# Optimization experiments

Measured on AMD Instinct MI355X. Metric: run time of the kernel, lower is better.

## Reference

```python
import jax, jax.numpy as jnp
import numpy as np

HEAD = 64

PARAM_NAMES = ['x_r','x_w','x_k','x_v','x_a','x_g','w0','w1','w2','a0','a1','a2',
               'v0','v1','v2','g1','g2','k_k','k_a','r_k','W_r','W_k','W_v','W_o',
               'ln_x_w','ln_x_b','ln1_w','ln1_b','ln2_w','ln2_b','c_x_k','W_ck','W_cv']


def token_shift(x):
    # previous token, zero-padded at t=0 (stateless shift state)
    return jnp.pad(x, ((0, 0), (1, 0), (0, 0)))[:, :-1]


def layer_norm(x, w, b, eps=1e-5):
    m = jnp.mean(x, -1, keepdims=True)
    v = jnp.mean(jnp.square(x - m), -1, keepdims=True)
    return (x - m) * jax.lax.rsqrt(v + eps) * w + b


def group_norm_heads(x, w, b, H, eps=64e-5):
    # GroupNorm(H, C) as used by RWKV7 ln_x (eps = head_size * 1e-5)
    B, T, C = x.shape
    xh = x.reshape(B, T, H, C // H)
    m = jnp.mean(xh, -1, keepdims=True)
    v = jnp.mean(jnp.square(xh - m), -1, keepdims=True)
    xh = (xh - m) * jax.lax.rsqrt(v + eps)
    return xh.reshape(B, T, C) * w + b


def wkv7(r, w, k, v, a, b):
    # r,w,k,v,a,b: [B,T,H,N]; w is per-channel decay in (0,1)
    # S_t = S_{t-1} * diag(w_t) + (S_{t-1} @ a_t) b_t^T + v_t k_t^T ; y_t = S_t @ r_t
    B, T, H, N = r.shape
    def step(S, inp):
        r_t, w_t, k_t, v_t, a_t, b_t = inp
        sa = jnp.einsum('bhij,bhj->bhi', S, a_t)
        S = S * w_t[:, :, None, :] + sa[..., None] * b_t[:, :, None, :] + v_t[..., None] * k_t[:, :, None, :]
        y = jnp.einsum('bhij,bhj->bhi', S, r_t)
        return S, y
    xs = tuple(jnp.moveaxis(t, 1, 0) for t in (r, w, k, v, a, b))
    S0 = jnp.zeros((B, H, N, N), r.dtype)
    _, ys = jax.lax.scan(step, S0, xs)
    return jnp.moveaxis(ys, 0, 1)


def time_mix(x, v_first, p, is_first_layer):
    B, T, C = x.shape
    H, N = C // HEAD, HEAD
    xx = token_shift(x) - x
    xr = x + xx * p['x_r']; xw = x + xx * p['x_w']; xk = x + xx * p['x_k']
    xv = x + xx * p['x_v']; xa = x + xx * p['x_a']; xg = x + xx * p['x_g']
    r = xr @ p['W_r']
    w = -jax.nn.softplus(-(p['w0'] + jnp.tanh(xw @ p['w1']) @ p['w2'])) - 0.5
    k = xk @ p['W_k']
    v = xv @ p['W_v']
    if is_first_layer:
        v_first = v
    else:
        v = v + (v_first - v) * jax.nn.sigmoid(p['v0'] + (xv @ p['v1']) @ p['v2'])
    a = jax.nn.sigmoid(p['a0'] + (xa @ p['a1']) @ p['a2'])  # in-context learning rate
    g = jax.nn.sigmoid(xg @ p['g1']) @ p['g2']
    kk = (k * p['k_k']).reshape(B, T, H, N)
    kk = kk / jnp.maximum(jnp.linalg.norm(kk, axis=-1, keepdims=True), 1e-12)
    k = k * (1.0 + (a - 1.0) * p['k_a'])
    decay = jnp.exp(-jnp.exp(w)).reshape(B, T, H, N)
    rh = r.reshape(B, T, H, N)
    kh = k.reshape(B, T, H, N)
    vh = v.reshape(B, T, H, N)
    ah = a.reshape(B, T, H, N)
    y = wkv7(rh, decay, kh, vh, -kk, kk * ah).reshape(B, T, C)
    y = group_norm_heads(y, p['ln_x_w'], p['ln_x_b'], H)
    bonus = jnp.sum(rh * kh * p['r_k'], -1, keepdims=True) * vh
    y = y + bonus.reshape(B, T, C)
    return (y * g) @ p['W_o'], v_first


def channel_mix(x, p):
    xx = token_shift(x) - x
    k = x + xx * p['c_x_k']
    k = jnp.square(jax.nn.relu(k @ p['W_ck']))
    return k @ p['W_cv']


def encoder_forward(x, params):
    L = params['W_r'].shape[0]
    v_first = None
    for i in range(L):
        p = {n: params[n][i] for n in PARAM_NAMES}
        att, v_first = time_mix(layer_norm(x, p['ln1_w'], p['ln1_b']), v_first, p, i == 0)
        x = x + att
        x = x + channel_mix(layer_norm(x, p['ln2_w'], p['ln2_b']), p)
    return x


def setup_inputs() -> dict:
    key = jax.random.key(0)
    L, B, T, C = 6, 2, 512, 768
    H, N = C // HEAD, HEAD
    Dw, Da, Dv, Dg, F = 64, 64, 32, 128, 4 * C
    keys = iter(jax.random.split(key, 48))
    def rn(shape, s):
        return jax.random.normal(next(keys), shape, jnp.float32) * s
    def ru(shape):
        return jax.random.uniform(next(keys), shape, jnp.float32)
    inp = {
        'x': rn((B, T, C), 1.0),
        'x_r': ru((L, C)), 'x_w': ru((L, C)), 'x_k': ru((L, C)),
        'x_v': ru((L, C)), 'x_a': ru((L, C)), 'x_g': ru((L, C)),
        'w0': rn((L, C), 0.3), 'w1': rn((L, C, Dw), 0.02), 'w2': rn((L, Dw, C), 0.02),
        'a0': rn((L, C), 0.1), 'a1': rn((L, C, Da), 0.02), 'a2': rn((L, Da, C), 0.02),
        'v0': rn((L, C), 0.1), 'v1': rn((L, C, Dv), 0.02), 'v2': rn((L, Dv, C), 0.02),
        'g1': rn((L, C, Dg), 0.02), 'g2': rn((L, Dg, C), 0.02),
        'k_k': 0.85 + rn((L, C), 0.05), 'k_a': 1.0 + rn((L, C), 0.05),
        'r_k': rn((L, H, N), 0.1),
        'W_r': rn((L, C, C), 0.02), 'W_k': rn((L, C, C), 0.02),
        'W_v': rn((L, C, C), 0.02), 'W_o': rn((L, C, C), 0.02),
        'ln_x_w': 1.0 + rn((L, C), 0.05), 'ln_x_b': rn((L, C), 0.05),
        'ln1_w': 1.0 + rn((L, C), 0.05), 'ln1_b': rn((L, C), 0.05),
        'ln2_w': 1.0 + rn((L, C), 0.05), 'ln2_b': rn((L, C), 0.05),
        'c_x_k': ru((L, C)),
        'W_ck': rn((L, C, F), 0.02), 'W_cv': rn((L, F, C), 0.02),
    }
    return inp


def reference(x, x_r, x_w, x_k, x_v, x_a, x_g, w0, w1, w2, a0, a1, a2, v0, v1, v2,
              g1, g2, k_k, k_a, r_k, W_r, W_k, W_v, W_o, ln_x_w, ln_x_b,
              ln1_w, ln1_b, ln2_w, ln2_b, c_x_k, W_ck, W_cv):
    params = dict(zip(PARAM_NAMES, (x_r, x_w, x_k, x_v, x_a, x_g, w0, w1, w2, a0, a1, a2,
                                    v0, v1, v2, g1, g2, k_k, k_a, r_k, W_r, W_k, W_v, W_o,
                                    ln_x_w, ln_x_b, ln1_w, ln1_b, ln2_w, ln2_b, c_x_k, W_ck, W_cv)))
    return encoder_forward(x, params)
```

## Files before the change

### kernel.cpp

```cpp
#include <hip/hip_runtime.h>
#include <hip/hip_bf16.h>
#include <math.h>

#define LAYERS 6
#define BBATCH 2
#define TT 512
#define CC 768
#define HH 12
#define MT (BBATCH*TT)
#define FF (4*CC)
#define LCH 32
#define NC (TT/LCH)
#define BH (BBATCH*HH)
#define SPAD 65

typedef __hip_bfloat16 bf16;
typedef __bf16 bf16x8 __attribute__((ext_vector_type(8)));
typedef __bf16 bf16x4 __attribute__((ext_vector_type(4)));
typedef float f32x4 __attribute__((ext_vector_type(4)));

__device__ inline bf16 f2b(float f) { return __float2bfloat16(f); }
__device__ inline __bf16 f2bb(float f) {
    __hip_bfloat16 h = __float2bfloat16(f);
    return __builtin_bit_cast(__bf16, h);
}
__device__ inline float bb2f(__bf16 h) {
    return __bfloat162float(__builtin_bit_cast(__hip_bfloat16, h));
}


__global__ __launch_bounds__(256) void copy_f(float* __restrict__ dst, const float* __restrict__ src) {
    size_t i = (size_t)blockIdx.x * 256 + threadIdx.x;
    dst[i] = src[i];
}


__global__ __launch_bounds__(256) void ln_shift_kernel(const float* __restrict__ x,
                                                       const float* __restrict__ w,
                                                       const float* __restrict__ b,
                                                       bf16* __restrict__ out) {
    int row = blockIdx.x;
    int t = row % TT;
    const float* xr = x + (size_t)row * CC;
    const float* xp = xr - CC;
    int tid = threadIdx.x;
    float c0 = xr[tid], c1 = xr[tid + 256], c2 = xr[tid + 512];
    float p0 = 0.f, p1 = 0.f, p2 = 0.f;
    if (t > 0) { p0 = xp[tid]; p1 = xp[tid + 256]; p2 = xp[tid + 512]; }
    float s  = c0 + c1 + c2, q  = c0 * c0 + c1 * c1 + c2 * c2;
    float sp = p0 + p1 + p2, qp = p0 * p0 + p1 * p1 + p2 * p2;
    for (int m = 1; m < 64; m <<= 1) {
        s += __shfl_xor(s, m); q += __shfl_xor(q, m);
        sp += __shfl_xor(sp, m); qp += __shfl_xor(qp, m);
    }
    __shared__ float rs[4], rq[4], rsp[4], rqp[4];
    int wid = tid >> 6;
    if ((tid & 63) == 0) { rs[wid] = s; rq[wid] = q; rsp[wid] = sp; rqp[wid] = qp; }
    __syncthreads();
    s  = rs[0] + rs[1] + rs[2] + rs[3];   q  = rq[0] + rq[1] + rq[2] + rq[3];
    sp = rsp[0] + rsp[1] + rsp[2] + rsp[3]; qp = rqp[0] + rqp[1] + rqp[2] + rqp[3];
    float meanC = s * (1.f / CC);
    float invC  = rsqrtf(q * (1.f / CC) - meanC * meanC + 1e-5f);
    float meanP = sp * (1.f / CC);
    float invP  = rsqrtf(qp * (1.f / CC) - meanP * meanP + 1e-5f);
    bf16* orow = out + (size_t)row * 1536;
    float cv[3] = {c0, c1, c2};
    float pv[3] = {p0, p1, p2};
#pragma unroll
    for (int j = 0; j < 3; ++j) {
        int cc = tid + j * 256;
        float lnc = (cv[j] - meanC) * invC * w[cc] + b[cc];
        float lnp = (t > 0) ? (pv[j] - meanP) * invP * w[cc] + b[cc] : 0.f;
        orow[cc] = f2b(lnc);
        orow[768 + cc] = f2b(lnp - lnc);
    }
}


struct CEntry { const float* W; const float* mix; bf16* dst; int Ksrc, Nsrc, Npad, Kdst, bstart; };
struct CArgs { CEntry e[14]; };

__global__ __launch_bounds__(256) void convert_weights(CArgs ca) {
    int bid = blockIdx.x;
    int idx = 0;
#pragma unroll
    for (int i = 1; i < 14; ++i) if (bid >= ca.e[i].bstart) idx = i;
    CEntry E = ca.e[idx];
    int t = bid - E.bstart;
    int ntN = E.Npad >> 5;
    int tn = (t % ntN) * 32, tk = (t / ntN) * 32;
    __shared__ float tile[32][33];
    int c = threadIdx.x & 31, r0 = threadIdx.x >> 5;
    int ks = tk;
    const float* mixp = nullptr;
    if (tk >= E.Ksrc) { ks = tk - E.Ksrc; mixp = E.mix; }
#pragma unroll
    for (int i = 0; i < 4; ++i) {
        int r = r0 + i * 8;
        float v = (tn + c < E.Nsrc) ? E.W[(size_t)(ks + r) * E.Nsrc + tn + c] : 0.f;
        if (mixp) v *= mixp[ks + r];
        tile[r][c] = v;
    }
    __syncthreads();
#pragma unroll
    for (int i = 0; i < 4; ++i) {
        int r = r0 + i * 8;
        E.dst[(size_t)(tn + r) * E.Kdst + tk + c] = f2b(tile[c][r]);
    }
}


struct EpiG {
    float* outF; bf16* outH;
    const float* p1; const float* p2;
    int epi, ld, ntrue;
};
struct EpiArgs { EpiG g[7]; int nb[8]; };

__device__ inline void epi_store(const EpiG& E, size_t idx, int lc, float v) {
    switch (E.epi) {
        case 0: E.outF[idx] = v; break;
        case 1: E.outH[idx] = f2b(v); break;
        case 2: E.outH[idx] = f2b(tanhf(v)); break;
        case 3: E.outH[idx] = f2b(1.f / (1.f + expf(-v))); break;
        case 4: { float t = fmaxf(v, 0.f); E.outH[idx] = f2b(t * t); } break;
        case 5: E.outF[idx] += v; break;
        case 6: { float z = E.p1[lc] + v; float nz = -z;
                  float sp = (nz > 20.f) ? nz : log1pf(expf(nz));
                  E.outF[idx] = expf(-expf(-sp - 0.5f)); } break;
        case 7: E.outF[idx] = 1.f / (1.f + expf(-(E.p1[lc] + v))); break;
        case 8: { float vv = E.outF[idx];
                  float s = 1.f / (1.f + expf(-(E.p1[lc] + v)));
                  E.outF[idx] = vv + (E.p2[idx] - vv) * s; } break;
    }
}


template<int BM, int BN>
__global__ __launch_bounds__(256) void gemm_multi(const __bf16* __restrict__ A,
                                                  const __bf16* __restrict__ Bt,
                                                  int K, EpiArgs ea) {
    constexpr int FM = BM / 32, FN = BN / 32;
    constexpr int ABYTES = BM * 64;
    constexpr int TOT = (BM + BN) * 64;
    constexpr int NCHUNK = TOT / 4096;
    __shared__ __align__(16) char smem[2][TOT];
    int tid = threadIdx.x;
    int lane = tid & 63, wid = tid >> 6;
    int bm = blockIdx.y * BM, bn = blockIdx.x * BN;
    int wm = (wid >> 1) * (BM / 2), wn = (wid & 1) * (BN / 2);
    f32x4 acc[FM][FN];
#pragma unroll
    for (int i = 0; i < FM; ++i)
#pragma unroll
        for (int j = 0; j < FN; ++j) acc[i][j] = (f32x4){0.f, 0.f, 0.f, 0.f};

    int nk = K >> 5;
    auto stage = [&](int buf, int k0) {
        char* sb = &smem[buf][0];
#pragma unroll
        for (int c = 0; c < NCHUNK; ++c) {
            int d = c * 4096 + tid * 16;
            int isB = d >= ABYTES;
            int dd = isB ? d - ABYTES : d;
            int row = dd >> 6;
            int u = (dd >> 4) & 3;
            int su = u ^ (row & 3);
            const __bf16* src = isB ? (Bt + (size_t)(bn + row) * K + k0 + su * 8)
                                    : (A  + (size_t)(bm + row) * K + k0 + su * 8);
            char* ldst = sb + c * 4096 + (tid & 192) * 16;
            __builtin_amdgcn_global_load_lds(
                (const __attribute__((address_space(1))) unsigned int*)src,
                (__attribute__((address_space(3))) unsigned int*)ldst, 16, 0, 0);
        }
    };

    stage(0, 0);
    __syncthreads();
    for (int t = 0; t < nk; ++t) {
        if (t + 1 < nk) stage((t + 1) & 1, (t + 1) * 32);
        const char* sA = &smem[t & 1][0];
        const char* sB = &smem[t & 1][ABYTES];
        int u = lane >> 4, r0 = lane & 15;
        bf16x8 af[FM], bfr[FN];
#pragma unroll
        for (int i = 0; i < FM; ++i) {
            int row = wm + i * 16 + r0;
            int su = u ^ (row & 3);
            af[i] = *(const bf16x8*)(sA + row * 64 + su * 16);
        }
#pragma unroll
        for (int j = 0; j < FN; ++j) {
            int row = wn + j * 16 + r0;
            int su = u ^ (row & 3);
            bfr[j] = *(const bf16x8*)(sB + row * 64 + su * 16);
        }
#pragma unroll
        for (int i = 0; i < FM; ++i)
#pragma unroll
            for (int j = 0; j < FN; ++j)
                acc[i][j] = __builtin_amdgcn_mfma_f32_16x16x32_bf16(af[i], bfr[j], acc[i][j], 0, 0, 0);
        __syncthreads();
    }

    int gid = 0;
#pragma unroll 1
    while (bn >= ea.nb[gid + 1]) ++gid;
    EpiG E = ea.g[gid];
    int colBase = ea.nb[gid];
#pragma unroll
    for (int i = 0; i < FM; ++i) {
#pragma unroll
        for (int j = 0; j < FN; ++j) {
#pragma unroll
            for (int q = 0; q < 4; ++q) {
                int gm = bm + wm + i * 16 + (lane >> 4) * 4 + q;
                int lc = bn + wn + j * 16 + (lane & 15) - colBase;
                if (lc < E.ntrue)
                    epi_store(E, (size_t)gm * E.ld + lc, lc, acc[i][j][q]);
            }
        }
    }
}


struct G2G { const __bf16* A; const __bf16* Bt; float* outF; const float* p1; const float* p2; int K; int epi; };
struct G2Args { G2G g[4]; };

template<int BM, int BN>
__global__ __launch_bounds__(256) void gemm_g2(G2Args ga) {
    G2G G = ga.g[blockIdx.z];
    const __bf16* A = G.A;
    const __bf16* Bt = G.Bt;
    int K = G.K;
    constexpr int FM = BM / 32, FN = BN / 32;
    constexpr int ABYTES = BM * 64;
    constexpr int TOT = (BM + BN) * 64;
    constexpr int NCHUNK = TOT / 4096;
    __shared__ __align__(16) char smem[2][TOT];
    int tid = threadIdx.x;
    int lane = tid & 63, wid = tid >> 6;
    int bm = blockIdx.y * BM, bn = blockIdx.x * BN;
    int wm = (wid >> 1) * (BM / 2), wn = (wid & 1) * (BN / 2);
    f32x4 acc[FM][FN];
#pragma unroll
    for (int i = 0; i < FM; ++i)
#pragma unroll
        for (int j = 0; j < FN; ++j) acc[i][j] = (f32x4){0.f, 0.f, 0.f, 0.f};

    int nk = K >> 5;
    auto stage = [&](int buf, int k0) {
        char* sb = &smem[buf][0];
#pragma unroll
        for (int c = 0; c < NCHUNK; ++c) {
            int d = c * 4096 + tid * 16;
            int isB = d >= ABYTES;
            int dd = isB ? d - ABYTES : d;
            int row = dd >> 6;
            int u = (dd >> 4) & 3;
            int su = u ^ (row & 3);
            const __bf16* src = isB ? (Bt + (size_t)(bn + row) * K + k0 + su * 8)
                                    : (A  + (size_t)(bm + row) * K + k0 + su * 8);
            char* ldst = sb + c * 4096 + (tid & 192) * 16;
            __builtin_amdgcn_global_load_lds(
                (const __attribute__((address_space(1))) unsigned int*)src,
                (__attribute__((address_space(3))) unsigned int*)ldst, 16, 0, 0);
        }
    };

    stage(0, 0);
    __syncthreads();
    for (int t = 0; t < nk; ++t) {
        if (t + 1 < nk) stage((t + 1) & 1, (t + 1) * 32);
        const char* sA = &smem[t & 1][0];
        const char* sB = &smem[t & 1][ABYTES];
        int u = lane >> 4, r0 = lane & 15;
        bf16x8 af[FM], bfr[FN];
#pragma unroll
        for (int i = 0; i < FM; ++i) {
            int row = wm + i * 16 + r0;
            int su = u ^ (row & 3);
            af[i] = *(const bf16x8*)(sA + row * 64 + su * 16);
        }
#pragma unroll
        for (int j = 0; j < FN; ++j) {
            int row = wn + j * 16 + r0;
            int su = u ^ (row & 3);
            bfr[j] = *(const bf16x8*)(sB + row * 64 + su * 16);
        }
#pragma unroll
        for (int i = 0; i < FM; ++i)
#pragma unroll
            for (int j = 0; j < FN; ++j)
                acc[i][j] = __builtin_amdgcn_mfma_f32_16x16x32_bf16(af[i], bfr[j], acc[i][j], 0, 0, 0);
        __syncthreads();
    }

    EpiG E;
    E.outF = G.outF; E.outH = nullptr; E.p1 = G.p1; E.p2 = G.p2;
    E.epi = G.epi; E.ld = 768; E.ntrue = 768;
#pragma unroll
    for (int i = 0; i < FM; ++i) {
#pragma unroll
        for (int j = 0; j < FN; ++j) {
#pragma unroll
            for (int q = 0; q < 4; ++q) {
                int gm = bm + wm + i * 16 + (lane >> 4) * 4 + q;
                int lc = bn + wn + j * 16 + (lane & 15);
                epi_store(E, (size_t)gm * 768 + lc, lc, acc[i][j][q]);
            }
        }
    }
}


__global__ __launch_bounds__(256) void chunkA_kernel(
    const float* __restrict__ r, const float* __restrict__ wd,
    const float* __restrict__ kraw, const float* __restrict__ av_,
    const float* __restrict__ v,
    const float* __restrict__ kkw, const float* __restrict__ kaw,
    float* __restrict__ kupd,
    float* __restrict__ yintra, float* __restrict__ zrO,
    __bf16* __restrict__ mtHi, __bf16* __restrict__ mtLo,
    float* __restrict__ zcO) {
    int c = blockIdx.x, bh = blockIdx.y;
    int b = bh / HH, h = bh % HH;
    __shared__ float Di[LCH][SPAD];
    __shared__ float Ah[LCH][SPAD];
    __shared__ float Bh[LCH][SPAD];
    __shared__ float Kh[LCH][SPAD];
    __shared__ float Rh[LCH][SPAD];
    __shared__ float Vt[LCH][SPAD];
    __shared__ float Qm[LCH][SPAD];
    __shared__ float Gba[LCH][LCH], Gka[LCH][LCH], Grb[LCH][LCH], Grk[LCH][LCH];
    int tid = threadIdx.x;
    int n = tid & 63, tq = tid >> 6;
    size_t base = ((size_t)(b * TT + c * LCH)) * CC + h * 64 + n;
    int cvec = h * 64 + n;
    float kkwv = kkw[cvec], kawv = kaw[cvec];
#pragma unroll
    for (int e = 0; e < 8; ++e) {
        int t = tq * 8 + e;
        size_t off = base + (size_t)t * CC;
        float kr = kraw[off];
        float aval = av_[off];
        float kk0 = kr * kkwv;
        float ss = kk0 * kk0;
        for (int m = 1; m < 64; m <<= 1) ss += __shfl_xor(ss, m);
        float rinv = 1.f / fmaxf(sqrtf(ss), 1e-12f);
        float kkv = kk0 * rinv;
        float ku = kr * (1.f + (aval - 1.f) * kawv);
        kupd[off] = ku;
        Di[t][n] = wd[off];
        Ah[t][n] = -kkv;
        Bh[t][n] = kkv * aval;
        Kh[t][n] = ku;
        Rh[t][n] = r[off];
        Vt[t][n] = v[off];
    }
    __syncthreads();
    if (tid < 64) {
        float d = 1.f;
        for (int t = 0; t < LCH; ++t) { d *= Di[t][tid]; Di[t][tid] = d; }
    }
    __syncthreads();
#pragma unroll
    for (int e = 0; e < 8; ++e) {
        int t = tq * 8 + e;
        float di = Di[t][n];
        float dp = (t == 0) ? 1.f : Di[t - 1][n];
        float inv = 1.f / di;
        Ah[t][n] *= dp;
        Bh[t][n] *= inv;
        Kh[t][n] *= inv;
        Rh[t][n] *= di;
    }
    __syncthreads();
    {
        int tp = tid >> 4, sp = tid & 15;
        int t0 = 2 * tp, s0 = 2 * sp;
        float gba00 = 0.f, gba01 = 0.f, gba10 = 0.f, gba11 = 0.f;
        float gka00 = 0.f, gka01 = 0.f, gka10 = 0.f, gka11 = 0.f;
        float grb00 = 0.f, grb01 = 0.f, grb10 = 0.f, grb11 = 0.f;
        float grk00 = 0.f, grk01 = 0.f, grk10 = 0.f, grk11 = 0.f;
#pragma unroll 4
        for (int j = 0; j < 64; ++j) {
            float a0 = Ah[t0][j], a1 = Ah[t0 + 1][j];
            float r0 = Rh[t0][j], r1 = Rh[t0 + 1][j];
            float b0 = Bh[s0][j], b1 = Bh[s0 + 1][j];
            float k0 = Kh[s0][j], k1 = Kh[s0 + 1][j];
            gba00 = fmaf(a0, b0, gba00); gba01 = fmaf(a0, b1, gba01);
            gba10 = fmaf(a1, b0, gba10); gba11 = fmaf(a1, b1, gba11);
            gka00 = fmaf(a0, k0, gka00); gka01 = fmaf(a0, k1, gka01);
            gka10 = fmaf(a1, k0, gka10); gka11 = fmaf(a1, k1, gka11);
            grb00 = fmaf(r0, b0, grb00); grb01 = fmaf(r0, b1, grb01);
            grb10 = fmaf(r1, b0, grb10); grb11 = fmaf(r1, b1, grb11);
            grk00 = fmaf(r0, k0, grk00); grk01 = fmaf(r0, k1, grk01);
            grk10 = fmaf(r1, k0, grk10); grk11 = fmaf(r1, k1, grk11);
        }
#pragma unroll
        for (int dt = 0; dt < 2; ++dt) {
            int t = t0 + dt;
#pragma unroll
            for (int ds = 0; ds < 2; ++ds) {
                int s = s0 + ds;
                float vba = dt ? (ds ? gba11 : gba10) : (ds ? gba01 : gba00);
                float vka = dt ? (ds ? gka11 : gka10) : (ds ? gka01 : gka00);
                float vrb = dt ? (ds ? grb11 : grb10) : (ds ? grb01 : grb00);
                float vrk = dt ? (ds ? grk11 : grk10) : (ds ? grk01 : grk00);
                Gba[t][s] = (s < t)  ? vba : 0.f;
                Gka[t][s] = (s < t)  ? vka : 0.f;
                Grb[t][s] = (s <= t) ? vrb : 0.f;
                Grk[t][s] = (s <= t) ? vrk : 0.f;
            }
        }
    }
    __syncthreads();
    {
        float acc[8];
#pragma unroll
        for (int e = 0; e < 8; ++e) acc[e] = 0.f;
        for (int s = 0; s < LCH; ++s) {
            float vs = Vt[s][n];
#pragma unroll
            for (int e = 0; e < 8; ++e)
                acc[e] = fmaf(Gka[tq * 8 + e][s], vs, acc[e]);
        }
#pragma unroll
        for (int e = 0; e < 8; ++e) Qm[tq * 8 + e][n] = acc[e];
    }
    __syncthreads();
    if (tq == 0) {
        for (int t = 1; t < LCH; ++t) {
            float acc = Ah[t][n];
            for (int s = 0; s < t; ++s) acc = fmaf(Gba[t][s], Ah[s][n], acc);
            Ah[t][n] = acc;
        }
    } else if (tq == 1) {
        for (int t = 1; t < LCH; ++t) {
            float acc = Qm[t][n];
            for (int s = 0; s < t; ++s) acc = fmaf(Gba[t][s], Qm[s][n], acc);
            Qm[t][n] = acc;
        }
    }
    __syncthreads();
    size_t obase = ((size_t)(bh * NC + c)) * LCH * 64;
    {
        float accY[8], accZ[8];
#pragma unroll
        for (int e = 0; e < 8; ++e) { accY[e] = 0.f; accZ[e] = Rh[tq * 8 + e][n]; }
        for (int s = 0; s < LCH; ++s) {
            float vs = Vt[s][n], qs = Qm[s][n], us = Ah[s][n];
#pragma unroll
            for (int e = 0; e < 8; ++e) {
                int t = tq * 8 + e;
                float grk_ = Grk[t][s], grb_ = Grb[t][s];
                accY[e] = fmaf(grk_, vs, fmaf(grb_, qs, accY[e]));
                accZ[e] = fmaf(grb_, us, accZ[e]);
            }
        }
#pragma unroll
        for (int e = 0; e < 8; ++e) {
            int t = tq * 8 + e;
            yintra[obase + t * 64 + n] = accY[e];
            zrO[obase + t * 64 + n] = accZ[e];
        }
    }
    {
        int pi = tid >> 4, ni = tid & 15;
        float accM[4][4], accZc[4][4];
#pragma unroll
        for (int dp = 0; dp < 4; ++dp)
#pragma unroll
            for (int dn = 0; dn < 4; ++dn) { accM[dp][dn] = 0.f; accZc[dp][dn] = 0.f; }
        for (int s = 0; s < LCH; ++s) {
            float aa[4], vv[4], qq[4], bb[4], kk[4];
#pragma unroll
            for (int d = 0; d < 4; ++d) {
                aa[d] = Ah[s][4 * pi + d];
                vv[d] = Vt[s][4 * pi + d];
                qq[d] = Qm[s][4 * pi + d];
                bb[d] = Bh[s][4 * ni + d];
                kk[d] = Kh[s][4 * ni + d];
            }
#pragma unroll
            for (int dp = 0; dp < 4; ++dp)
#pragma unroll
                for (int dn = 0; dn < 4; ++dn) {
                    accM[dp][dn]  = fmaf(aa[dp], bb[dn], accM[dp][dn]);
                    accZc[dp][dn] = fmaf(vv[dp], kk[dn], fmaf(qq[dp], bb[dn], accZc[dp][dn]));
                }
        }
        size_t mbase = ((size_t)(bh * NC + c)) * 4096;
        float dl[4];
#pragma unroll
        for (int dn = 0; dn < 4; ++dn) dl[dn] = Di[LCH - 1][4 * ni + dn];
#pragma unroll
        for (int dp = 0; dp < 4; ++dp) {
            int p = 4 * pi + dp;
            f32x4 z4;
#pragma unroll
            for (int dn = 0; dn < 4; ++dn) z4[dn] = dl[dn] * accZc[dp][dn];
            *(f32x4*)(zcO + mbase + p * 64 + 4 * ni) = z4;
        }
#pragma unroll
        for (int dn = 0; dn < 4; ++dn) {
            int nn = 4 * ni + dn;
            float dlv = dl[dn];
            bf16x4 h4, l4;
#pragma unroll
            for (int dp = 0; dp < 4; ++dp) {
                int p = 4 * pi + dp;
                float mm = (accM[dp][dn] + ((p == nn) ? 1.f : 0.f)) * dlv;
                __bf16 hb = f2bb(mm);
                h4[dp] = hb;
                l4[dp] = f2bb(mm - bb2f(hb));
            }
            *(bf16x4*)(mtHi + mbase + (size_t)nn * 64 + 4 * pi) = h4;
            *(bf16x4*)(mtLo + mbase + (size_t)nn * 64 + 4 * pi) = l4;
        }
    }
}


__global__ __launch_bounds__(256) void chunkB1_kernel(
    const float* __restrict__ zc,
    const __bf16* __restrict__ mtHi,
    const __bf16* __restrict__ mtLo,
    float* __restrict__ schk) {
    int bh = blockIdx.x;
    int tid = threadIdx.x;
    int lane = tid & 63, w = tid >> 6;
    int r0 = lane & 15, u = lane >> 4;
    __shared__ __align__(16) float S[64][68];
    for (int i = tid; i < 64 * 68; i += 256) (&S[0][0])[i] = 0.f;
    const float* zbase = zc + (size_t)bh * NC * 4096;
    const __bf16* hbase = mtHi + (size_t)bh * NC * 4096;
    const __bf16* lbase = mtLo + (size_t)bh * NC * 4096;
    float* sbase = schk + (size_t)bh * NC * 4096;
    int arow = w * 16 + r0;

    bf16x8 mh[2][4][2], ml[2][4][2];
    f32x4 zf[2][4];
#pragma unroll
    for (int ct = 0; ct < 4; ++ct) {
#pragma unroll
        for (int ks = 0; ks < 2; ++ks) {
            size_t mo = (size_t)(ct * 16 + r0) * 64 + ks * 32 + u * 8;
            mh[0][ct][ks] = *(const bf16x8*)(hbase + mo);
            ml[0][ct][ks] = *(const bf16x8*)(lbase + mo);
        }
#pragma unroll
        for (int q = 0; q < 4; ++q)
            zf[0][ct][q] = zbase[(size_t)(w * 16 + u * 4 + q) * 64 + ct * 16 + r0];
    }
    __syncthreads();
#pragma unroll
    for (int c = 0; c < NC - 1; ++c) {
        constexpr int dummy = 0; (void)dummy;
        const int cb = c & 1;
        if (c + 1 < NC - 1) {
            const __bf16* hn = hbase + (size_t)(c + 1) * 4096;
            const __bf16* ln = lbase + (size_t)(c + 1) * 4096;
            const float* zn = zbase + (size_t)(c + 1) * 4096;
#pragma unroll
            for (int ct = 0; ct < 4; ++ct) {
#pragma unroll
                for (int ks = 0; ks < 2; ++ks) {
                    size_t mo = (size_t)(ct * 16 + r0) * 64 + ks * 32 + u * 8;
                    mh[cb ^ 1][ct][ks] = *(const bf16x8*)(hn + mo);
                    ml[cb ^ 1][ct][ks] = *(const bf16x8*)(ln + mo);
                }
#pragma unroll
                for (int q = 0; q < 4; ++q)
                    zf[cb ^ 1][ct][q] = zn[(size_t)(w * 16 + u * 4 + q) * 64 + ct * 16 + r0];
            }
        }
        bf16x8 ah[2], al[2];
#pragma unroll
        for (int ks = 0; ks < 2; ++ks) {
            f32x4 s0 = *(const f32x4*)&S[arow][ks * 32 + u * 8];
            f32x4 s1 = *(const f32x4*)&S[arow][ks * 32 + u * 8 + 4];
#pragma unroll
            for (int e = 0; e < 4; ++e) {
                __bf16 h0 = f2bb(s0[e]);
                ah[ks][e] = h0;
                al[ks][e] = f2bb(s0[e] - bb2f(h0));
                __bf16 h1 = f2bb(s1[e]);
                ah[ks][4 + e] = h1;
                al[ks][4 + e] = f2bb(s1[e] - bb2f(h1));
            }
        }
        f32x4 acc[4];
#pragma unroll
        for (int ct = 0; ct < 4; ++ct) {
            acc[ct] = zf[cb][ct];
#pragma unroll
            for (int ks = 0; ks < 2; ++ks) {
                acc[ct] = __builtin_amdgcn_mfma_f32_16x16x32_bf16(ah[ks], mh[cb][ct][ks], acc[ct], 0, 0, 0);
                acc[ct] = __builtin_amdgcn_mfma_f32_16x16x32_bf16(ah[ks], ml[cb][ct][ks], acc[ct], 0, 0, 0);
                acc[ct] = __builtin_amdgcn_mfma_f32_16x16x32_bf16(al[ks], mh[cb][ct][ks], acc[ct], 0, 0, 0);
            }
        }
        __syncthreads();
        float* cp = sbase + (size_t)(c + 1) * 4096;
#pragma unroll
        for (int ct = 0; ct < 4; ++ct) {
#pragma unroll
            for (int q = 0; q < 4; ++q) {
                int row = w * 16 + u * 4 + q;
                int col = ct * 16 + r0;
                S[row][col] = acc[ct][q];
                cp[(size_t)row * 64 + col] = acc[ct][q];
            }
        }
        __syncthreads();
    }
}


__global__ __launch_bounds__(256) void chunkY_kernel(
    const float* __restrict__ yintra, const float* __restrict__ zrI,
    const float* __restrict__ schk,
    const float* __restrict__ r, const float* __restrict__ kupd,
    const float* __restrict__ v, const float* __restrict__ g,
    const float* __restrict__ rk, const float* __restrict__ lw,
    const float* __restrict__ lb, bf16* __restrict__ out) {
    int c = blockIdx.x, bh = blockIdx.y;
    int b = bh / HH, h = bh % HH;
    __shared__ float Y[LCH][SPAD];
    __shared__ float Zr[LCH][SPAD];
    __shared__ float Sh[64][SPAD];
    int tid = threadIdx.x;
    int n = tid & 63, tq = tid >> 6;
    size_t obase = ((size_t)(bh * NC + c)) * LCH * 64;
#pragma unroll
    for (int e = 0; e < 8; ++e) {
        int idx = tid + e * 256;
        int row = idx >> 6, col = idx & 63;
        Y[row][col] = yintra[obase + idx];
        Zr[row][col] = zrI[obase + idx];
    }
    if (c > 0) {
        size_t sbase = ((size_t)(bh * NC + c)) * 4096;
#pragma unroll
        for (int e = 0; e < 16; ++e) {
            int idx = tid + e * 256;
            Sh[idx >> 6][idx & 63] = schk[sbase + idx];
        }
    }
    __syncthreads();
    if (c > 0) {
        float acc[8];
#pragma unroll
        for (int e = 0; e < 8; ++e) acc[e] = 0.f;
        for (int p = 0; p < 64; ++p) {
            float sv = Sh[n][p];
#pragma unroll
            for (int e = 0; e < 8; ++e)
                acc[e] = fmaf(Zr[tq * 8 + e][p], sv, acc[e]);
        }
#pragma unroll
        for (int e = 0; e < 8; ++e) Y[tq * 8 + e][n] += acc[e];
    }
    size_t rowbase = ((size_t)(b * TT + c * LCH)) * CC + h * 64 + n;
    float rkv = rk[h * 64 + n];
    float lwv = lw[h * 64 + n], lbv = lb[h * 64 + n];
#pragma unroll
    for (int e = 0; e < 8; ++e) {
        int t = tq * 8 + e;
        size_t off = rowbase + (size_t)t * CC;
        float yv = Y[t][n];
        float rv = r[off], kv = kupd[off], vv = v[off];
        float s1 = yv, s2 = yv * yv, s3 = rv * kv * rkv;
        for (int m = 1; m < 64; m <<= 1) {
            s1 += __shfl_xor(s1, m);
            s2 += __shfl_xor(s2, m);
            s3 += __shfl_xor(s3, m);
        }
        float mean = s1 * (1.f / 64.f);
        float var  = s2 * (1.f / 64.f) - mean * mean;
        float inv  = rsqrtf(var + 64e-5f);
        float val  = (yv - mean) * inv * lwv + lbv + s3 * vv;
        out[off] = f2b(val * g[off]);
    }
}


extern "C" void kernel_launch(void* const* d_in, const int* in_sizes, int n_in,
                              void* d_out, int out_size, void* d_ws, size_t ws_size,
                              hipStream_t stream) {
    (void)in_sizes; (void)n_in; (void)out_size;
    const float* x    = (const float*)d_in[0];
    const float* x_r  = (const float*)d_in[1];
    const float* x_w  = (const float*)d_in[2];
    const float* x_k  = (const float*)d_in[3];
    const float* x_v  = (const float*)d_in[4];
    const float* x_a  = (const float*)d_in[5];
    const float* x_g  = (const float*)d_in[6];
    const float* w0   = (const float*)d_in[7];
    const float* w1   = (const float*)d_in[8];
    const float* w2   = (const float*)d_in[9];
    const float* a0   = (const float*)d_in[10];
    const float* a1   = (const float*)d_in[11];
    const float* a2   = (const float*)d_in[12];
    const float* v0   = (const float*)d_in[13];
    const float* v1   = (const float*)d_in[14];
    const float* v2   = (const float*)d_in[15];
    const float* g1   = (const float*)d_in[16];
    const float* g2   = (const float*)d_in[17];
    const float* k_k  = (const float*)d_in[18];
    const float* k_a  = (const float*)d_in[19];
    const float* r_k  = (const float*)d_in[20];
    const float* W_r  = (const float*)d_in[21];
    const float* W_k  = (const float*)d_in[22];
    const float* W_v  = (const float*)d_in[23];
    const float* W_o  = (const float*)d_in[24];
    const float* ln_x_w = (const float*)d_in[25];
    const float* ln_x_b = (const float*)d_in[26];
    const float* ln1_w  = (const float*)d_in[27];
    const float* ln1_b  = (const float*)d_in[28];
    const float* ln2_w  = (const float*)d_in[29];
    const float* ln2_b  = (const float*)d_in[30];
    const float* c_x_k  = (const float*)d_in[31];
    const float* W_ck   = (const float*)d_in[32];
    const float* W_cv   = (const float*)d_in[33];

    const size_t MC = (size_t)MT * CC;
    char* wsb = (char*)d_ws;
    size_t woff = 0;
    auto alloc = [&](size_t bytes) -> void* {
        void* p = wsb + woff;
        woff += (bytes + 255) & ~(size_t)255;
        return p;
    };
    bf16* Bcat  = (bf16*)alloc((size_t)2624 * 1536 * 2);
    bf16* Bck   = (bf16*)alloc((size_t)3072 * 1536 * 2);
    bf16* w2t   = (bf16*)alloc((size_t)768 * 64 * 2);
    bf16* a2t   = (bf16*)alloc((size_t)768 * 64 * 2);
    bf16* v2t   = (bf16*)alloc((size_t)768 * 32 * 2);
    bf16* g2t   = (bf16*)alloc((size_t)768 * 128 * 2);
    bf16* Wo_t  = (bf16*)alloc((size_t)768 * 768 * 2);
    bf16* Wcv_t = (bf16*)alloc((size_t)768 * 3072 * 2);
    bf16* A1    = (bf16*)alloc((size_t)MT * 1536 * 2);
    float* rbuf  = (float*)alloc(MC * 4);
    float* kraw  = (float*)alloc(MC * 4);
    float* kupd  = (float*)alloc(MC * 4);
    float* vbuf  = (float*)alloc(MC * 4);
    float* vfirst= (float*)alloc(MC * 4);
    float* abuf  = (float*)alloc(MC * 4);
    float* dbuf  = (float*)alloc(MC * 4);
    float* gbuf  = (float*)alloc(MC * 4);
    bf16* w1o   = (bf16*)alloc((size_t)MT * 64 * 2);
    bf16* a1o   = (bf16*)alloc((size_t)MT * 64 * 2);
    bf16* v1o   = (bf16*)alloc((size_t)MT * 32 * 2);
    bf16* g1o   = (bf16*)alloc((size_t)MT * 128 * 2);
    bf16* hbuf  = (bf16*)alloc((size_t)MT * FF * 2);
    bf16* ghout = (bf16*)alloc(MC * 2);
    float* yintraW = (float*)alloc((size_t)BH * NC * LCH * 64 * 4);
    float* zrW     = (float*)alloc((size_t)BH * NC * LCH * 64 * 4);
    __bf16* mtHiW  = (__bf16*)alloc((size_t)BH * NC * 4096 * 2);
    __bf16* mtLoW  = (__bf16*)alloc((size_t)BH * NC * 4096 * 2);
    float* zcW     = (float*)alloc((size_t)BH * NC * 4096 * 4);
    float* schkW   = (float*)alloc((size_t)BH * NC * 4096 * 4);
    if (woff > ws_size) return;

    float* xcur = (float*)d_out;
    copy_f<<<MC / 256, 256, 0, stream>>>(xcur, x);

    for (int l = 0; l < LAYERS; ++l) {
        size_t oC = (size_t)l * CC;
        float* vptr = (l == 0) ? vfirst : vbuf;

        CArgs ca;
        ca.e[0]  = {W_r  + (size_t)l * 589824, x_r + oC, Bcat,               768, 768, 768, 1536, 0};
        ca.e[1]  = {W_k  + (size_t)l * 589824, x_k + oC, Bcat + (size_t)768  * 1536, 768, 768, 768, 1536, 0};
        ca.e[2]  = {W_v  + (size_t)l * 589824, x_v + oC, Bcat + (size_t)1536 * 1536, 768, 768, 768, 1536, 0};
        ca.e[3]  = {w1   + (size_t)l * 49152,  x_w + oC, Bcat + (size_t)2304 * 1536, 768, 64, 64, 1536, 0};
        ca.e[4]  = {a1   + (size_t)l * 49152,  x_a + oC, Bcat + (size_t)2368 * 1536, 768, 64, 64, 1536, 0};
        ca.e[5]  = {g1   + (size_t)l * 98304,  x_g + oC, Bcat + (size_t)2432 * 1536, 768, 128, 128, 1536, 0};
        ca.e[6]  = {v1   + (size_t)l * 24576,  x_v + oC, Bcat + (size_t)2560 * 1536, 768, 32, 64, 1536, 0};
        ca.e[7]  = {W_ck + (size_t)l * 2359296, c_x_k + oC, Bck, 768, 3072, 3072, 1536, 0};
        ca.e[8]  = {w2   + (size_t)l * 49152,  nullptr, w2t,   64, 768, 768, 64, 0};
        ca.e[9]  = {a2   + (size_t)l * 49152,  nullptr, a2t,   64, 768, 768, 64, 0};
        ca.e[10] = {v2   + (size_t)l * 24576,  nullptr, v2t,   32, 768, 768, 32, 0};
        ca.e[11] = {g2   + (size_t)l * 98304,  nullptr, g2t,  128, 768, 768, 128, 0};
        ca.e[12] = {W_o  + (size_t)l * 589824, nullptr, Wo_t, 768, 768, 768, 768, 0};
        ca.e[13] = {W_cv + (size_t)l * 2359296, nullptr, Wcv_t, 3072, 768, 768, 3072, 0};
        int btot = 0;
        for (int i = 0; i < 14; ++i) {
            ca.e[i].bstart = btot;
            btot += (ca.e[i].Npad >> 5) * (ca.e[i].Kdst >> 5);
        }
        convert_weights<<<btot, 256, 0, stream>>>(ca);

        ln_shift_kernel<<<MT, 256, 0, stream>>>(xcur, ln1_w + oC, ln1_b + oC, A1);

        EpiArgs e1;
        e1.g[0] = {rbuf,  nullptr, nullptr, nullptr, 0, 768, 768};
        e1.g[1] = {kraw,  nullptr, nullptr, nullptr, 0, 768, 768};
        e1.g[2] = {vptr,  nullptr, nullptr, nullptr, 0, 768, 768};
        e1.g[3] = {nullptr, w1o, nullptr, nullptr, 2, 64, 64};
        e1.g[4] = {nullptr, a1o, nullptr, nullptr, 1, 64, 64};
        e1.g[5] = {nullptr, g1o, nullptr, nullptr, 3, 128, 128};
        e1.g[6] = {nullptr, v1o, nullptr, nullptr, 1, 32, 32};
        int nb1[8] = {0, 768, 1536, 2304, 2368, 2432, 2560, 2624};
        for (int i = 0; i < 8; ++i) e1.nb[i] = nb1[i];
        gemm_multi<128, 64><<<dim3(41, 8), 256, 0, stream>>>((const __bf16*)A1, (const __bf16*)Bcat, 1536, e1);

        G2Args g2a;
        g2a.g[0] = {(const __bf16*)w1o, (const __bf16*)w2t, dbuf, w0 + oC, nullptr, 64, 6};
        g2a.g[1] = {(const __bf16*)a1o, (const __bf16*)a2t, abuf, a0 + oC, nullptr, 64, 7};
        g2a.g[2] = {(const __bf16*)g1o, (const __bf16*)g2t, gbuf, nullptr, nullptr, 128, 0};
        g2a.g[3] = {(const __bf16*)v1o, (const __bf16*)v2t, vbuf, v0 + oC, vfirst, 32, 8};
        gemm_g2<128, 64><<<dim3(12, 8, (l == 0) ? 3 : 4), 256, 0, stream>>>(g2a);

        chunkA_kernel<<<dim3(NC, BH), 256, 0, stream>>>(rbuf, dbuf, kraw, abuf, vptr,
                                                        k_k + oC, k_a + oC, kupd,
                                                        yintraW, zrW, mtHiW, mtLoW, zcW);
        chunkB1_kernel<<<BH, 256, 0, stream>>>(zcW, mtHiW, mtLoW, schkW);
        chunkY_kernel<<<dim3(NC, BH), 256, 0, stream>>>(yintraW, zrW, schkW,
                                                        rbuf, kupd, vptr, gbuf,
                                                        r_k + (size_t)l * 768,
                                                        ln_x_w + oC, ln_x_b + oC, ghout);

        EpiArgs eo;
        eo.g[0] = {xcur, nullptr, nullptr, nullptr, 5, 768, 768};
        eo.nb[0] = 0; for (int i = 1; i < 8; ++i) eo.nb[i] = 1 << 30;
        eo.nb[1] = 768;
        gemm_multi<64, 64><<<dim3(12, 16), 256, 0, stream>>>((const __bf16*)ghout, (const __bf16*)Wo_t, 768, eo);

        ln_shift_kernel<<<MT, 256, 0, stream>>>(xcur, ln2_w + oC, ln2_b + oC, A1);

        EpiArgs ec;
        ec.g[0] = {nullptr, hbuf, nullptr, nullptr, 4, 3072, 3072};
        ec.nb[0] = 0; for (int i = 1; i < 8; ++i) ec.nb[i] = 1 << 30;
        ec.nb[1] = 3072;
        gemm_multi<128, 64><<<dim3(48, 8), 256, 0, stream>>>((const __bf16*)A1, (const __bf16*)Bck, 1536, ec);

        EpiArgs ev;
        ev.g[0] = {xcur, nullptr, nullptr, nullptr, 5, 768, 768};
        ev.nb[0] = 0; for (int i = 1; i < 8; ++i) ev.nb[i] = 1 << 30;
        ev.nb[1] = 768;
        gemm_multi<64, 64><<<dim3(12, 16), 256, 0, stream>>>((const __bf16*)hbuf, (const __bf16*)Wcv_t, 3072, ev);
    }
}
```

Baseline: 1.483 ms.

## Deepen GEMM K-tile to 64 with 8-way LDS swizzle and XCD-aware block remap

The gemm_multi kernel now stages 64-wide K slices instead of 32, which halves the number of barrier-separated iterations and issues two MFMA k-steps per stage. Its LDS XOR swizzle is widened to 8 slots to match the 128-byte rows. Workgroup IDs are remapped so consecutive tiles land on the same XCD chiplet, aiming for better L2 reuse. The second GEMM variant gets a different swizzle pattern (row>>1) to cut LDS bank conflicts. Shared memory per block doubles, which may lower occupancy.

```diff
diff --git a/kernel.cpp b/kernel.cpp
--- a/kernel.cpp
+++ b/kernel.cpp
@@ -141,13 +141,17 @@
                                                   const __bf16* __restrict__ Bt,
                                                   int K, EpiArgs ea) {
     constexpr int FM = BM / 32, FN = BN / 32;
-    constexpr int ABYTES = BM * 64;
-    constexpr int TOT = (BM + BN) * 64;
+    constexpr int ABYTES = BM * 128;
+    constexpr int TOT = (BM + BN) * 128;
     constexpr int NCHUNK = TOT / 4096;
     __shared__ __align__(16) char smem[2][TOT];
     int tid = threadIdx.x;
     int lane = tid & 63, wid = tid >> 6;
-    int bm = blockIdx.y * BM, bn = blockIdx.x * BN;
+    int nwg = gridDim.x * gridDim.y;
+    int orig = blockIdx.y * gridDim.x + blockIdx.x;
+    int qq = nwg >> 3, rr = nwg & 7, xc = orig & 7, oo = orig >> 3;
+    int swz = (xc < rr ? xc * (qq + 1) : rr * (qq + 1) + (xc - rr) * qq) + oo;
+    int bn = (swz % gridDim.x) * BN, bm = (swz / gridDim.x) * BM;
     int wm = (wid >> 1) * (BM / 2), wn = (wid & 1) * (BN / 2);
     f32x4 acc[FM][FN];
 #pragma unroll
@@ -155,7 +159,7 @@
 #pragma unroll
         for (int j = 0; j < FN; ++j) acc[i][j] = (f32x4){0.f, 0.f, 0.f, 0.f};
 
-    int nk = K >> 5;
+    int nk = K >> 6;
     auto stage = [&](int buf, int k0) {
         char* sb = &smem[buf][0];
 #pragma unroll
@@ -163,9 +167,9 @@
             int d = c * 4096 + tid * 16;
             int isB = d >= ABYTES;
             int dd = isB ? d - ABYTES : d;
-            int row = dd >> 6;
-            int u = (dd >> 4) & 3;
-            int su = u ^ (row & 3);
+            int row = dd >> 7;
+            int slot = (dd >> 4) & 7;
+            int su = slot ^ (row & 7);
             const __bf16* src = isB ? (Bt + (size_t)(bn + row) * K + k0 + su * 8)
                                     : (A  + (size_t)(bm + row) * K + k0 + su * 8);
             char* ldst = sb + c * 4096 + (tid & 192) * 16;
@@ -178,28 +182,33 @@
     stage(0, 0);
     __syncthreads();
     for (int t = 0; t < nk; ++t) {
-        if (t + 1 < nk) stage((t + 1) & 1, (t + 1) * 32);
+        if (t + 1 < nk) stage((t + 1) & 1, (t + 1) * 64);
         const char* sA = &smem[t & 1][0];
         const char* sB = &smem[t & 1][ABYTES];
         int u = lane >> 4, r0 = lane & 15;
-        bf16x8 af[FM], bfr[FN];
-#pragma unroll
-        for (int i = 0; i < FM; ++i) {
-            int row = wm + i * 16 + r0;
-            int su = u ^ (row & 3);
-            af[i] = *(const bf16x8*)(sA + row * 64 + su * 16);
-        }
-#pragma unroll
-        for (int j = 0; j < FN; ++j) {
-            int row = wn + j * 16 + r0;
-            int su = u ^ (row & 3);
-            bfr[j] = *(const bf16x8*)(sB + row * 64 + su * 16);
-        }
-#pragma unroll
-        for (int i = 0; i < FM; ++i)
-#pragma unroll
-            for (int j = 0; j < FN; ++j)
-                acc[i][j] = __builtin_amdgcn_mfma_f32_16x16x32_bf16(af[i], bfr[j], acc[i][j], 0, 0, 0);
+        bf16x8 af[2][FM], bfr[2][FN];
+#pragma unroll
+        for (int ks = 0; ks < 2; ++ks) {
+#pragma unroll
+            for (int i = 0; i < FM; ++i) {
+                int row = wm + i * 16 + r0;
+                int slot = (ks * 4 + u) ^ (row & 7);
+                af[ks][i] = *(const bf16x8*)(sA + row * 128 + slot * 16);
+            }
+#pragma unroll
+            for (int j = 0; j < FN; ++j) {
+                int row = wn + j * 16 + r0;
+                int slot = (ks * 4 + u) ^ (row & 7);
+                bfr[ks][j] = *(const bf16x8*)(sB + row * 128 + slot * 16);
+            }
+        }
+#pragma unroll
+        for (int ks = 0; ks < 2; ++ks)
+#pragma unroll
+            for (int i = 0; i < FM; ++i)
+#pragma unroll
+                for (int j = 0; j < FN; ++j)
+                    acc[i][j] = __builtin_amdgcn_mfma_f32_16x16x32_bf16(af[ks][i], bfr[ks][j], acc[i][j], 0, 0, 0);
         __syncthreads();
     }
 
@@ -258,7 +267,7 @@
             int dd = isB ? d - ABYTES : d;
             int row = dd >> 6;
             int u = (dd >> 4) & 3;
-            int su = u ^ (row & 3);
+            int su = u ^ ((row >> 1) & 3);
             const __bf16* src = isB ? (Bt + (size_t)(bn + row) * K + k0 + su * 8)
                                     : (A  + (size_t)(bm + row) * K + k0 + su * 8);
             char* ldst = sb + c * 4096 + (tid & 192) * 16;
@@ -279,13 +288,13 @@
 #pragma unroll
         for (int i = 0; i < FM; ++i) {
             int row = wm + i * 16 + r0;
-            int su = u ^ (row & 3);
+            int su = u ^ ((row >> 1) & 3);
             af[i] = *(const bf16x8*)(sA + row * 64 + su * 16);
         }
 #pragma unroll
         for (int j = 0; j < FN; ++j) {
             int row = wn + j * 16 + r0;
-            int su = u ^ (row & 3);
+            int su = u ^ ((row >> 1) & 3);
             bfr[j] = *(const bf16x8*)(sB + row * 64 + su * 16);
         }
 #pragma unroll
@@ -557,7 +566,6 @@
     __syncthreads();
 #pragma unroll
     for (int c = 0; c < NC - 1; ++c) {
-        constexpr int dummy = 0; (void)dummy;
         const int cb = c & 1;
         if (c + 1 < NC - 1) {
             const __bf16* hn = hbase + (size_t)(c + 1) * 4096;
```

New measurement: 1.410 ms. 1.05x faster.
